# Optimization experiments

Measured on AMD Instinct MI355X. Metric: run time of the kernel, lower is better.

The kernel has to match this reference:

```python
import jax, jax.numpy as jnp
import numpy as np

B = 16384          # batch
WIDTH = 128        # nodes per DAG layer
N_HIDDEN = 30      # hidden layers
DEG = 16           # in-degree of each non-source node
N_WL = N_HIDDEN + 1            # weighted layers (hidden + sink layer) = 31
N_NODES = (N_WL + 1) * WIDTH   # 32 layers * 128 = 4096 total DAG nodes


def setup_inputs() -> dict:
    rng = np.random.default_rng(0)
    # Mask M per layer: (preds+bias, layer_width); bias row (last) is all ones.
    masks = np.zeros((N_WL, WIDTH + 1, WIDTH), np.float32)
    masks[:, -1, :] = 1.0
    for l in range(N_WL):
        for j in range(WIDTH):
            rows = rng.choice(WIDTH, size=DEG, replace=False)
            masks[l, rows, j] = 1.0
    # kaiming_uniform_(a=sqrt(5)) on (nnz,1) tensors has fan_in=1 -> U(-1,1) per nnz entry.
    weights = (rng.uniform(-1.0, 1.0, masks.shape).astype(np.float32)) * masks
    # Layered DAG: preds of weighted layer l are exactly the nodes of layer l (global ids l*W..(l+1)*W).
    preds_idx = np.stack([np.arange(l * WIDTH, (l + 1) * WIDTH) for l in range(N_WL)]).astype(np.int32)
    layers_idx = preds_idx + WIDTH  # nodes written by weighted layer l
    x = jax.random.normal(jax.random.key(0), (B, WIDTH), jnp.float32)
    return {
        "x": x,
        "weights": jnp.asarray(weights),
        "masks": jnp.asarray(masks),
        "preds_idx": jnp.asarray(preds_idx),
        "layers_idx": jnp.asarray(layers_idx),
    }


def reference(x, weights, masks, preds_idx, layers_idx):
    b = x.shape[0]
    act = jnp.zeros((b, N_NODES), x.dtype)
    act = act.at[:, :WIDTH].set(x)           # activations[:, sources] = x
    ones = jnp.ones((b, 1), x.dtype)         # bias column (bias=True)
    # dropout p=0.0 -> identity

    def step(act, layer_inputs):
        W, M, preds, layer = layer_inputs
        h = jnp.concatenate([jnp.take(act, preds, axis=1), ones], axis=1)  # [b, preds+1]
        out = jax.nn.relu(h @ (M * W))                                     # [b, width]
        return act.at[:, layer].set(out), None

    act, _ = jax.lax.scan(step, act, (weights, masks, preds_idx, layers_idx))
    sinks = layers_idx[-1]
    return jnp.take(act, sinks, axis=1)       # activations[:, sinks]
```

## Files before the change

### kernel.cpp

```cpp
#include <hip/hip_runtime.h>
#include <stdint.h>

#define NWL 31

typedef __attribute__((ext_vector_type(8))) short short8;
typedef __attribute__((ext_vector_type(4))) short short4v;
typedef __attribute__((ext_vector_type(4))) float f32x4;

#define WCOMP 32768
#define WLAYER 65536
#define WS_W_BYTES (NWL * WLAYER)

#define LDS_WBUF0 0
#define LDS_WBUF1 65536
#define LDS_ACTH  131072
#define LDS_ACTL  147456
#define LDS_TOTAL 163840

__device__ __forceinline__ uint16_t f2bf(float f) {
  uint32_t u = __builtin_bit_cast(uint32_t, f);
  u += 0x7FFFu + ((u >> 16) & 1u);
  return (uint16_t)(u >> 16);
}
__device__ __forceinline__ float bf2f(uint16_t b) {
  return __builtin_bit_cast(float, (uint32_t)b << 16);
}

__device__ __forceinline__ void gload_lds16(const void* g, void* l) {
  __builtin_amdgcn_global_load_lds(
      (const __attribute__((address_space(1))) uint32_t*)g,
      (__attribute__((address_space(3))) uint32_t*)l, 16, 0, 0);
}

__global__ __launch_bounds__(512)
void prep_weights(const float* __restrict__ W, const float* __restrict__ M,
                  char* __restrict__ wsW, float* __restrict__ wsB) {
  const int l    = blockIdx.x >> 2;
  const int kk   = blockIdx.x & 3;
  const int nt   = threadIdx.x >> 6;
  const int lane = threadIdx.x & 63;
  const int kbase = kk * 32 + ((lane >> 4) << 3);
  const int n     = (nt << 4) + (lane & 15);
  const float* Wl = W + l * 129 * 128;
  const float* Ml = M + l * 129 * 128;
  short8 vh, vl;
#pragma unroll
  for (int i = 0; i < 8; ++i) {
    const int k = kbase + i;
    const float v = Wl[k * 128 + n] * Ml[k * 128 + n];
    const uint16_t h = f2bf(v);
    vh[i] = (short)h;
    vl[i] = (short)f2bf(v - bf2f(h));
  }
  char* base = wsW + l * WLAYER;
  const int frag = ((kk * 8 + nt) * 64 + lane) * 16;
  *(short8*)(base + frag)         = vh;
  *(short8*)(base + WCOMP + frag) = vl;
  if (kk == 0 && threadIdx.x < 128) {
    const int t = threadIdx.x;
    wsB[l * 128 + t] = Wl[128 * 128 + t] * Ml[128 * 128 + t];
  }
}

__global__ __launch_bounds__(512, 2)
void dag_mlp(const float* __restrict__ x, const char* __restrict__ wsW,
             const float* __restrict__ wsB, float* __restrict__ out) {
  extern __shared__ char lds[];
  const int tid  = threadIdx.x;
  const int lane = tid & 63;
  const int wv   = tid >> 6;
  const int wm   = wv >> 2;
  const int wn   = wv & 3;
  const int l16  = lane & 15;
  const int g4   = lane >> 4;
  const int r0   = blockIdx.x << 6;

  {
    const char* g = wsW;
#pragma unroll
    for (int r = 0; r < 8; ++r) {
      const int off = r * 8192 + wv * 1024;
      gload_lds16(g + off + lane * 16, lds + LDS_WBUF0 + off);
    }
  }
#pragma unroll
  for (int it = 0; it < 4; ++it) {
    const int idx = tid + it * 512;
    const int row = idx >> 5;
    const int k4  = idx & 31;
    const f32x4 v = *(const f32x4*)(x + (size_t)(r0 + row) * 128 + k4 * 4);
    short4v hv, lv;
#pragma unroll
    for (int c = 0; c < 4; ++c) {
      const uint16_t h = f2bf(v[c]);
      hv[c] = (short)h;
      lv[c] = (short)f2bf(v[c] - bf2f(h));
    }
    const int off = row * 256 + (((k4 >> 1) ^ (row & 7)) << 4) + ((k4 & 1) << 3);
    *(short4v*)(lds + LDS_ACTH + off) = hv;
    *(short4v*)(lds + LDS_ACTL + off) = lv;
  }
  __syncthreads();

  f32x4 acc[2][2];

  for (int l = 0; l < NWL; ++l) {
    const int cur = l & 1;
    if (l + 1 < NWL) {
      const char* g = wsW + (size_t)(l + 1) * WLAYER;
      const int dstbase = cur ? LDS_WBUF0 : LDS_WBUF1;
#pragma unroll
      for (int r = 0; r < 8; ++r) {
        const int off = r * 8192 + wv * 1024;
        gload_lds16(g + off + lane * 16, lds + dstbase + off);
      }
    }
#pragma unroll
    for (int fc = 0; fc < 2; ++fc) {
      const float bv = wsB[l * 128 + wn * 32 + fc * 16 + l16];
      f32x4 t = {bv, bv, bv, bv};
      acc[0][fc] = t;
      acc[1][fc] = t;
    }
    short8 aH[2][4], aL[2][4];
#pragma unroll
    for (int fr = 0; fr < 2; ++fr) {
      const int arow = wm * 32 + fr * 16 + l16;
#pragma unroll
      for (int kk = 0; kk < 4; ++kk) {
        const int off = arow * 256 + ((((kk << 2) + g4) ^ (arow & 7)) << 4);
        aH[fr][kk] = *(const short8*)(lds + LDS_ACTH + off);
        aL[fr][kk] = *(const short8*)(lds + LDS_ACTL + off);
      }
    }
    const int wbase = cur ? LDS_WBUF1 : LDS_WBUF0;
#pragma unroll
    for (int kk = 0; kk < 4; ++kk) {
      short8 bH[2], bL[2];
#pragma unroll
      for (int fc = 0; fc < 2; ++fc) {
        const int foff = wbase + (((kk * 8 + wn * 2 + fc) * 64 + lane) << 4);
        bH[fc] = *(const short8*)(lds + foff);
        bL[fc] = *(const short8*)(lds + WCOMP + foff);
      }
#pragma unroll
      for (int fr = 0; fr < 2; ++fr)
#pragma unroll
        for (int fc = 0; fc < 2; ++fc)
          acc[fr][fc] = __builtin_amdgcn_mfma_f32_16x16x32_bf16(aH[fr][kk], bH[fc], acc[fr][fc], 0, 0, 0);
#pragma unroll
      for (int fr = 0; fr < 2; ++fr)
#pragma unroll
        for (int fc = 0; fc < 2; ++fc)
          acc[fr][fc] = __builtin_amdgcn_mfma_f32_16x16x32_bf16(aL[fr][kk], bH[fc], acc[fr][fc], 0, 0, 0);
#pragma unroll
      for (int fr = 0; fr < 2; ++fr)
#pragma unroll
        for (int fc = 0; fc < 2; ++fc)
          acc[fr][fc] = __builtin_amdgcn_mfma_f32_16x16x32_bf16(aH[fr][kk], bL[fc], acc[fr][fc], 0, 0, 0);
    }
    __syncthreads();
    if (l == NWL - 1) {
#pragma unroll
      for (int fr = 0; fr < 2; ++fr)
#pragma unroll
        for (int fc = 0; fc < 2; ++fc) {
          const int col = wn * 32 + fc * 16 + l16;
#pragma unroll
          for (int i = 0; i < 4; ++i) {
            const int row = r0 + wm * 32 + fr * 16 + g4 * 4 + i;
            out[(size_t)row * 128 + col] = fmaxf(acc[fr][fc][i], 0.0f);
          }
        }
    } else {
#pragma unroll
      for (int fr = 0; fr < 2; ++fr)
#pragma unroll
        for (int fc = 0; fc < 2; ++fc) {
          const int col = wn * 32 + fc * 16 + l16;
#pragma unroll
          for (int i = 0; i < 4; ++i) {
            const int row = wm * 32 + fr * 16 + g4 * 4 + i;
            const float v = fmaxf(acc[fr][fc][i], 0.0f);
            const uint16_t h  = f2bf(v);
            const uint16_t lo = f2bf(v - bf2f(h));
            const int off = row * 256 + (((col >> 3) ^ (row & 7)) << 4) + ((col & 7) << 1);
            *(uint16_t*)(lds + LDS_ACTH + off) = h;
            *(uint16_t*)(lds + LDS_ACTL + off) = lo;
          }
        }
      __syncthreads();
    }
  }
}

extern "C" void kernel_launch(void* const* d_in, const int* in_sizes, int n_in,
                              void* d_out, int out_size, void* d_ws, size_t ws_size,
                              hipStream_t stream) {
  const float* x = (const float*)d_in[0];
  const float* W = (const float*)d_in[1];
  const float* M = (const float*)d_in[2];
  char*  wsW = (char*)d_ws;
  float* wsB = (float*)((char*)d_ws + WS_W_BYTES);
  float* out = (float*)d_out;

  (void)hipFuncSetAttribute((const void*)dag_mlp,
                            hipFuncAttributeMaxDynamicSharedMemorySize, LDS_TOTAL);

  hipLaunchKernelGGL(prep_weights, dim3(NWL * 4), dim3(512), 0, stream, W, M, wsW, wsB);
  hipLaunchKernelGGL(dag_mlp, dim3(256), dim3(512), LDS_TOTAL, stream, x, wsW, wsB, out);
}
```

Before: 146.6 us.

## Pack hi/lo bf16 activation pairs into one LDS word with truncation split

Activations are now stored as one interleaved 32-bit word per element, holding the truncated-bf16 high part and the bf16 residual, instead of two separate hi and lo arrays. Each epilogue element then needs one 32-bit LDS store rather than two 16-bit stores, and the A-operand fragments are rebuilt from the packed words with v_perm byte permutes. Bias is added in the epilogue instead of seeding the accumulators, and LDS offsets are precomputed outside the layer loop. The split now truncates instead of rounding, so the hi part is slightly less accurate, and the extra permutes add ALU work on the load side.

```diff
diff --git a/kernel.cpp b/kernel.cpp
--- a/kernel.cpp
+++ b/kernel.cpp
@@ -4,8 +4,8 @@
 #define NWL 31
 
 typedef __attribute__((ext_vector_type(8))) short short8;
-typedef __attribute__((ext_vector_type(4))) short short4v;
 typedef __attribute__((ext_vector_type(4))) float f32x4;
+typedef __attribute__((ext_vector_type(4))) uint32_t u32x4;
 
 #define WCOMP 32768
 #define WLAYER 65536
@@ -13,8 +13,7 @@
 
 #define LDS_WBUF0 0
 #define LDS_WBUF1 65536
-#define LDS_ACTH  131072
-#define LDS_ACTL  147456
+#define LDS_ACT   131072
 #define LDS_TOTAL 163840
 
 __device__ __forceinline__ uint16_t f2bf(float f) {
@@ -24,6 +23,21 @@
 }
 __device__ __forceinline__ float bf2f(uint16_t b) {
   return __builtin_bit_cast(float, (uint32_t)b << 16);
+}
+
+__device__ __forceinline__ uint32_t perm_hihi(uint32_t hi, uint32_t lo) {
+#if __has_builtin(__builtin_amdgcn_perm)
+  return __builtin_amdgcn_perm(hi, lo, 0x07060302u);
+#else
+  return (hi & 0xFFFF0000u) | (lo >> 16);
+#endif
+}
+__device__ __forceinline__ uint32_t perm_lolo(uint32_t hi, uint32_t lo) {
+#if __has_builtin(__builtin_amdgcn_perm)
+  return __builtin_amdgcn_perm(hi, lo, 0x05040100u);
+#else
+  return (hi << 16) | (lo & 0xFFFFu);
+#endif
 }
 
 __device__ __forceinline__ void gload_lds16(const void* g, void* l) {
@@ -75,101 +89,148 @@
   const int g4   = lane >> 4;
   const int r0   = blockIdx.x << 6;
 
-  {
-    const char* g = wsW;
-#pragma unroll
-    for (int r = 0; r < 8; ++r) {
-      const int off = r * 8192 + wv * 1024;
-      gload_lds16(g + off + lane * 16, lds + LDS_WBUF0 + off);
-    }
-  }
+#pragma unroll
+  for (int r = 0; r < 8; ++r) {
+    const int off = r * 8192 + wv * 1024;
+    gload_lds16(wsW + off + lane * 16, lds + LDS_WBUF0 + off);
+  }
+
 #pragma unroll
   for (int it = 0; it < 4; ++it) {
     const int idx = tid + it * 512;
     const int row = idx >> 5;
-    const int k4  = idx & 31;
-    const f32x4 v = *(const f32x4*)(x + (size_t)(r0 + row) * 128 + k4 * 4);
-    short4v hv, lv;
+    const int cq  = idx & 31;
+    const f32x4 v = *(const f32x4*)(x + (size_t)(r0 + row) * 128 + cq * 4);
+    u32x4 w;
 #pragma unroll
     for (int c = 0; c < 4; ++c) {
-      const uint16_t h = f2bf(v[c]);
-      hv[c] = (short)h;
-      lv[c] = (short)f2bf(v[c] - bf2f(h));
-    }
-    const int off = row * 256 + (((k4 >> 1) ^ (row & 7)) << 4) + ((k4 & 1) << 3);
-    *(short4v*)(lds + LDS_ACTH + off) = hv;
-    *(short4v*)(lds + LDS_ACTL + off) = lv;
-  }
+      const uint32_t u  = __builtin_bit_cast(uint32_t, v[c]);
+      const float    hi = __builtin_bit_cast(float, u & 0xFFFF0000u);
+      const uint32_t ur = __builtin_bit_cast(uint32_t, v[c] - hi);
+      w[c] = perm_hihi(ur, u);
+    }
+    const int off = row * 512 + ((cq ^ (row & 7)) << 4);
+    *(u32x4*)(lds + LDS_ACT + off) = w;
+  }
+
+  int aoff[2][4][2];
+#pragma unroll
+  for (int fr = 0; fr < 2; ++fr) {
+    const int arow = wm * 32 + fr * 16 + l16;
+#pragma unroll
+    for (int kk = 0; kk < 4; ++kk) {
+      const int g0 = kk * 8 + g4 * 2;
+      aoff[fr][kk][0] = arow * 512 + (((g0    ) ^ (arow & 7)) << 4);
+      aoff[fr][kk][1] = arow * 512 + (((g0 + 1) ^ (arow & 7)) << 4);
+    }
+  }
+  int boff[4][2];
+#pragma unroll
+  for (int kk = 0; kk < 4; ++kk)
+#pragma unroll
+    for (int fc = 0; fc < 2; ++fc)
+      boff[kk][fc] = (((kk * 8 + wn * 2 + fc) * 64 + lane) << 4);
+  int eoff[2][2][4];
+#pragma unroll
+  for (int fr = 0; fr < 2; ++fr)
+#pragma unroll
+    for (int fc = 0; fc < 2; ++fc) {
+      const int col = wn * 32 + fc * 16 + l16;
+#pragma unroll
+      for (int i = 0; i < 4; ++i) {
+        const int row = wm * 32 + fr * 16 + g4 * 4 + i;
+        eoff[fr][fc][i] = row * 512 + (((col >> 2) ^ (row & 7)) << 4) + ((col & 3) << 2);
+      }
+    }
+  const float* biasp = wsB + wn * 32 + l16;
+
   __syncthreads();
 
-  f32x4 acc[2][2];
-
+  int wsel = 0;
   for (int l = 0; l < NWL; ++l) {
-    const int cur = l & 1;
     if (l + 1 < NWL) {
       const char* g = wsW + (size_t)(l + 1) * WLAYER;
-      const int dstbase = cur ? LDS_WBUF0 : LDS_WBUF1;
+      const int dst = wsel ^ 65536;
 #pragma unroll
       for (int r = 0; r < 8; ++r) {
         const int off = r * 8192 + wv * 1024;
-        gload_lds16(g + off + lane * 16, lds + dstbase + off);
-      }
-    }
-#pragma unroll
-    for (int fc = 0; fc < 2; ++fc) {
-      const float bv = wsB[l * 128 + wn * 32 + fc * 16 + l16];
-      f32x4 t = {bv, bv, bv, bv};
-      acc[0][fc] = t;
-      acc[1][fc] = t;
-    }
-    short8 aH[2][4], aL[2][4];
-#pragma unroll
-    for (int fr = 0; fr < 2; ++fr) {
-      const int arow = wm * 32 + fr * 16 + l16;
+        gload_lds16(g + off + lane * 16, lds + dst + off);
+      }
+    }
+    const float bias0 = biasp[l * 128];
+    const float bias1 = biasp[l * 128 + 16];
+
+    u32x4 ah[2][4], al[2][4];
+#pragma unroll
+    for (int fr = 0; fr < 2; ++fr)
 #pragma unroll
       for (int kk = 0; kk < 4; ++kk) {
-        const int off = arow * 256 + ((((kk << 2) + g4) ^ (arow & 7)) << 4);
-        aH[fr][kk] = *(const short8*)(lds + LDS_ACTH + off);
-        aL[fr][kk] = *(const short8*)(lds + LDS_ACTL + off);
-      }
-    }
-    const int wbase = cur ? LDS_WBUF1 : LDS_WBUF0;
+        const u32x4 p0 = *(const u32x4*)(lds + LDS_ACT + aoff[fr][kk][0]);
+        const u32x4 p1 = *(const u32x4*)(lds + LDS_ACT + aoff[fr][kk][1]);
+        ah[fr][kk][0] = perm_lolo(p0[1], p0[0]);
+        ah[fr][kk][1] = perm_lolo(p0[3], p0[2]);
+        ah[fr][kk][2] = perm_lolo(p1[1], p1[0]);
+        ah[fr][kk][3] = perm_lolo(p1[3], p1[2]);
+        al[fr][kk][0] = perm_hihi(p0[1], p0[0]);
+        al[fr][kk][1] = perm_hihi(p0[3], p0[2]);
+        al[fr][kk][2] = perm_hihi(p1[1], p1[0]);
+        al[fr][kk][3] = perm_hihi(p1[3], p1[2]);
+      }
+
+    f32x4 acc[2][2];
+#pragma unroll
+    for (int fr = 0; fr < 2; ++fr)
+#pragma unroll
+      for (int fc = 0; fc < 2; ++fc) {
+        f32x4 z = {0.f, 0.f, 0.f, 0.f};
+        acc[fr][fc] = z;
+      }
+
 #pragma unroll
     for (int kk = 0; kk < 4; ++kk) {
       short8 bH[2], bL[2];
 #pragma unroll
       for (int fc = 0; fc < 2; ++fc) {
-        const int foff = wbase + (((kk * 8 + wn * 2 + fc) * 64 + lane) << 4);
-        bH[fc] = *(const short8*)(lds + foff);
-        bL[fc] = *(const short8*)(lds + WCOMP + foff);
-      }
+        const char* p = lds + wsel + boff[kk][fc];
+        bH[fc] = *(const short8*)(p);
+        bL[fc] = *(const short8*)(p + WCOMP);
+      }
+#pragma unroll
+      for (int fr = 0; fr < 2; ++fr) {
+        const short8 aH = __builtin_bit_cast(short8, ah[fr][kk]);
+#pragma unroll
+        for (int fc = 0; fc < 2; ++fc)
+          acc[fr][fc] = __builtin_amdgcn_mfma_f32_16x16x32_bf16(aH, bH[fc], acc[fr][fc], 0, 0, 0);
+      }
+#pragma unroll
+      for (int fr = 0; fr < 2; ++fr) {
+        const short8 aL = __builtin_bit_cast(short8, al[fr][kk]);
+#pragma unroll
+        for (int fc = 0; fc < 2; ++fc)
+          acc[fr][fc] = __builtin_amdgcn_mfma_f32_16x16x32_bf16(aL, bH[fc], acc[fr][fc], 0, 0, 0);
+      }
+#pragma unroll
+      for (int fr = 0; fr < 2; ++fr) {
+        const short8 aH = __builtin_bit_cast(short8, ah[fr][kk]);
+#pragma unroll
+        for (int fc = 0; fc < 2; ++fc)
+          acc[fr][fc] = __builtin_amdgcn_mfma_f32_16x16x32_bf16(aH, bL[fc], acc[fr][fc], 0, 0, 0);
+      }
+    }
+
+    __syncthreads();
+
+    if (l == NWL - 1) {
 #pragma unroll
       for (int fr = 0; fr < 2; ++fr)
 #pragma unroll
-        for (int fc = 0; fc < 2; ++fc)
-          acc[fr][fc] = __builtin_amdgcn_mfma_f32_16x16x32_bf16(aH[fr][kk], bH[fc], acc[fr][fc], 0, 0, 0);
-#pragma unroll
-      for (int fr = 0; fr < 2; ++fr)
-#pragma unroll
-        for (int fc = 0; fc < 2; ++fc)
-          acc[fr][fc] = __builtin_amdgcn_mfma_f32_16x16x32_bf16(aL[fr][kk], bH[fc], acc[fr][fc], 0, 0, 0);
-#pragma unroll
-      for (int fr = 0; fr < 2; ++fr)
-#pragma unroll
-        for (int fc = 0; fc < 2; ++fc)
-          acc[fr][fc] = __builtin_amdgcn_mfma_f32_16x16x32_bf16(aH[fr][kk], bL[fc], acc[fr][fc], 0, 0, 0);
-    }
-    __syncthreads();
-    if (l == NWL - 1) {
-#pragma unroll
-      for (int fr = 0; fr < 2; ++fr)
-#pragma unroll
         for (int fc = 0; fc < 2; ++fc) {
+          const float bias = fc ? bias1 : bias0;
           const int col = wn * 32 + fc * 16 + l16;
 #pragma unroll
           for (int i = 0; i < 4; ++i) {
             const int row = r0 + wm * 32 + fr * 16 + g4 * 4 + i;
-            out[(size_t)row * 128 + col] = fmaxf(acc[fr][fc][i], 0.0f);
+            out[(size_t)row * 128 + col] = fmaxf(acc[fr][fc][i] + bias, 0.0f);
           }
         }
     } else {
@@ -177,19 +238,18 @@
       for (int fr = 0; fr < 2; ++fr)
 #pragma unroll
         for (int fc = 0; fc < 2; ++fc) {
-          const int col = wn * 32 + fc * 16 + l16;
+          const float bias = fc ? bias1 : bias0;
 #pragma unroll
           for (int i = 0; i < 4; ++i) {
-            const int row = wm * 32 + fr * 16 + g4 * 4 + i;
-            const float v = fmaxf(acc[fr][fc][i], 0.0f);
-            const uint16_t h  = f2bf(v);
-            const uint16_t lo = f2bf(v - bf2f(h));
-            const int off = row * 256 + (((col >> 3) ^ (row & 7)) << 4) + ((col & 7) << 1);
-            *(uint16_t*)(lds + LDS_ACTH + off) = h;
-            *(uint16_t*)(lds + LDS_ACTL + off) = lo;
+            const float v = fmaxf(acc[fr][fc][i] + bias, 0.0f);
+            const uint32_t u  = __builtin_bit_cast(uint32_t, v);
+            const float    hi = __builtin_bit_cast(float, u & 0xFFFF0000u);
+            const uint32_t ur = __builtin_bit_cast(uint32_t, v - hi);
+            *(uint32_t*)(lds + LDS_ACT + eoff[fr][fc][i]) = perm_hihi(ur, u);
           }
         }
       __syncthreads();
+      wsel ^= 65536;
     }
   }
 }
```

Result: faster. 130.2 us (-11.2%).
